# Kernel optimization log

Hardware: AMD Instinct MI355X
Metric: run time of the kernel (lower is better)

The kernel has to match this reference:

```python
import jax, jax.numpy as jnp
import numpy as np

B, S, D, H, DH = 2, 1024, 1024, 16, 64  # batch, seq, dim_model, heads, dim_head


def setup_inputs() -> dict:
    key = jax.random.key(0)
    ks = jax.random.split(key, 9)
    def W(k):
        return jax.random.normal(k, (D, D), jnp.float32) * 0.02
    z = jnp.zeros((D,), jnp.float32)
    return {
        "x": jax.random.normal(ks[0], (B, S, D), jnp.float32),
        "rel_pos_emb": jax.random.normal(ks[1], (B, S, D), jnp.float32),
        "padding_mask": jnp.zeros((B, S), jnp.int32),
        "Wq": W(ks[2]), "bq": z,
        "Wk": W(ks[3]), "bk": z,
        "Wv": W(ks[4]), "bv": z,
        "Wqr": W(ks[5]), "bqr": z,
        "Wkr": W(ks[6]), "bkr": z,
        "Wc": W(ks[7]), "bc": z,
    }


def reference(x, rel_pos_emb, padding_mask, Wq, bq, Wk, bk, Wv, bv, Wqr, bqr, Wkr, bkr, Wc, bc):
    b, s, d = x.shape

    def proj(t, W_, b_):  # (b,s,D) -> (b,H,s,DH)
        return (t @ W_.T + b_).reshape(b, s, H, DH).transpose(0, 2, 1, 3)

    q = proj(x, Wq, bq)
    k = proj(x, Wk, bk)
    v = proj(x, Wv, bv)
    qr = proj(rel_pos_emb, Wqr, bqr)
    kr = proj(rel_pos_emb, Wkr, bkr)

    # relative position index: clamp(i - j + MAX_REL_POS/2, 0, MAX_REL_POS-1), MAX_REL_POS = S
    idx = jnp.arange(s)
    pos = jnp.clip(idx[:, None] - idx[None, :] + s // 2, 0, s - 1)  # (s,s) int
    pos_b = jnp.broadcast_to(pos[None, None], (b, H, s, s))

    c2c = jnp.einsum('bhid,bhjd->bhij', q, k)
    c2p_att = jnp.einsum('bhid,bhjd->bhij', q, kr)
    c2p = jnp.take_along_axis(c2p_att, pos_b, axis=-1)   # gather along last dim
    p2c_att = jnp.einsum('bhid,bhjd->bhij', qr, k)
    p2c = jnp.take_along_axis(p2c_att, pos_b, axis=-2)   # gather along query dim

    scale = jnp.sqrt(jnp.asarray(3 * DH, jnp.float32))
    scores = (c2c + c2p + p2c) / scale
    scores = jnp.where(padding_mask[:, None, None, :] == 1, -jnp.inf, scores)
    attn = jax.nn.softmax(scores, axis=-1)  # dropout is identity in eval

    out = jnp.einsum('bhij,bhjd->bhid', attn, v)
    out = out.transpose(0, 2, 1, 3).reshape(b, s, H * DH)
    return out @ Wc.T + bc
```

## Files before the change

kernel.cpp:

```cpp
#include <hip/hip_runtime.h>

typedef unsigned short u16;
typedef unsigned int   u32;
typedef __bf16 bf16x8 __attribute__((ext_vector_type(8)));
typedef float  f32x4  __attribute__((ext_vector_type(4)));

__device__ __forceinline__ float b2f(u16 s) { return __uint_as_float(((u32)s) << 16); }
__device__ __forceinline__ u16 f2b(float f) {
  u32 x = __float_as_uint(f);
  return (u16)((x + 0x7FFFu + ((x >> 16) & 1u)) >> 16);
}

union U16x8 { uint4 u; u16 s[8]; };

__device__ __forceinline__ uint4 cvt8(const float4 a, const float4 b) {
  U16x8 r;
  r.s[0] = f2b(a.x); r.s[1] = f2b(a.y); r.s[2] = f2b(a.z); r.s[3] = f2b(a.w);
  r.s[4] = f2b(b.x); r.s[5] = f2b(b.y); r.s[6] = f2b(b.z); r.s[7] = f2b(b.w);
  return r.u;
}

typedef __attribute__((address_space(3))) u32 lds_u32;
typedef const __attribute__((address_space(1))) u32 glb_u32;
__device__ __forceinline__ void gld16(const u16* gp, u16* lp) {
  __builtin_amdgcn_global_load_lds((glb_u32*)gp, (lds_u32*)lp, 16, 0, 0);
}

struct CvtArgs { const float* s[8]; u16* d[8]; int n[8]; };

__global__ __launch_bounds__(256) void cvt_bf16(CvtArgs c) {
  const int t = blockIdx.y;
  const int i = (blockIdx.x * 256 + threadIdx.x) * 8;
  if (i >= c.n[t]) return;
  const float4 a = *(const float4*)(c.s[t] + i);
  const float4 b = *(const float4*)(c.s[t] + i + 4);
  *(uint4*)(c.d[t] + i) = cvt8(a, b);
}

struct GemmBArgs { const u16* A[5]; const u16* W[5]; const float* Bi[5]; void* C[5]; int vtz; };

template <int BN, bool OUT_F32>
__global__ __launch_bounds__(256) void gemm_lds(GemmBArgs g, int M, int N, int K) {
  const int z = blockIdx.z;
  const u16* __restrict__ A = g.A[z];
  const u16* __restrict__ W = g.W[z];
  const float* __restrict__ Bi = g.Bi[z];

  const int m0 = blockIdx.y * 128, n0 = blockIdx.x * BN;
  const int tid = threadIdx.x, wv = tid >> 6, lane = tid & 63;
  const int wm = wv >> 1, wn = wv & 1;
  const int lr = lane & 15, lq = lane >> 4;
  constexpr int NT = BN / 32;

  __shared__ u16 As[128 * 64];
  __shared__ u16 Ws[BN * 64];

  const f32x4 vzero = {0.f, 0.f, 0.f, 0.f};
  f32x4 acc[4][NT];
#pragma unroll
  for (int i = 0; i < 4; ++i)
#pragma unroll
    for (int j = 0; j < NT; ++j) acc[i][j] = vzero;

  const int srow = lane >> 3;
  const int sc   = (lane & 7) ^ srow;

  for (int kb = 0; kb < K; kb += 64) {
    __syncthreads();
#pragma unroll
    for (int t = 0; t < 4; ++t) {
      const u16* gp = A + (size_t)(m0 + t * 32 + wv * 8 + srow) * K + kb + sc * 8;
      gld16(gp, As + (t * 32 + wv * 8) * 64 + lane * 8);
    }
#pragma unroll
    for (int t = 0; t < NT; ++t) {
      const u16* gp = W + (size_t)(n0 + t * 32 + wv * 8 + srow) * K + kb + sc * 8;
      gld16(gp, Ws + (t * 32 + wv * 8) * 64 + lane * 8);
    }
    __syncthreads();
#pragma unroll
    for (int kk = 0; kk < 2; ++kk) {
      bf16x8 af[4], bw[NT];
#pragma unroll
      for (int mt = 0; mt < 4; ++mt) {
        const int row = wm * 64 + mt * 16 + lr;
        af[mt] = *(const bf16x8*)&As[row * 64 + (((kk << 2) | lq) ^ (row & 7)) * 8];
      }
#pragma unroll
      for (int nt = 0; nt < NT; ++nt) {
        const int row = wn * (BN / 2) + nt * 16 + lr;
        bw[nt] = *(const bf16x8*)&Ws[row * 64 + (((kk << 2) | lq) ^ (row & 7)) * 8];
      }
#pragma unroll
      for (int mt = 0; mt < 4; ++mt)
#pragma unroll
        for (int nt = 0; nt < NT; ++nt)
          acc[mt][nt] = __builtin_amdgcn_mfma_f32_16x16x32_bf16(af[mt], bw[nt], acc[mt][nt], 0, 0, 0);
    }
  }

#pragma unroll
  for (int mt = 0; mt < 4; ++mt) {
#pragma unroll
    for (int nt = 0; nt < NT; ++nt) {
      const int col = n0 + wn * (BN / 2) + nt * 16 + lr;
      const float bia = Bi[col];
      const int row0 = m0 + wm * 64 + mt * 16 + lq * 4;
      if (OUT_F32) {
#pragma unroll
        for (int r = 0; r < 4; ++r)
          ((float*)g.C[z])[(size_t)(row0 + r) * N + col] = acc[mt][nt][r] + bia;
      } else if (z == g.vtz) {
        ushort4 pk;
        pk.x = f2b(acc[mt][nt][0] + bia); pk.y = f2b(acc[mt][nt][1] + bia);
        pk.z = f2b(acc[mt][nt][2] + bia); pk.w = f2b(acc[mt][nt][3] + bia);
        const int bb = row0 >> 10, s0 = row0 & 1023;
        *(ushort4*)((u16*)g.C[z] + ((size_t)bb << 20) + ((size_t)col << 10) + s0) = pk;
      } else {
#pragma unroll
        for (int r = 0; r < 4; ++r)
          ((u16*)g.C[z])[(size_t)(row0 + r) * N + col] = f2b(acc[mt][nt][r] + bia);
      }
    }
  }
}

struct GemmArgs { const void* A[5]; const float* W[5]; const float* Bi[5]; void* C[5]; int vtz; };

template <bool A_F32, bool OUT_F32>
__global__ __launch_bounds__(256) void gemm5(GemmArgs g, int M, int N, int K) {
  const int z = blockIdx.z;
  const float* __restrict__ Wf = g.W[z];
  const float* __restrict__ Bi = g.Bi[z];

  const int m0 = blockIdx.y * 128, n0 = blockIdx.x * 128;
  const int tid = threadIdx.x;
  const int wv = tid >> 6, lane = tid & 63;
  const int wm = wv >> 1, wn = wv & 1;
  const int lr = lane & 15, lq = lane >> 4;

  __shared__ alignas(16) u16 As[128][64];
  __shared__ alignas(16) u16 Ws[128][64];

  const f32x4 vzero = {0.f, 0.f, 0.f, 0.f};
  f32x4 acc[4][4];
#pragma unroll
  for (int i = 0; i < 4; ++i)
#pragma unroll
    for (int j = 0; j < 4; ++j) acc[i][j] = vzero;

  const int srow = tid >> 1;
  const int sc0  = (tid & 1) * 32;
  const float* pw = Wf + (size_t)(n0 + srow) * K + sc0;
  const float* paf = A_F32 ? ((const float*)g.A[z] + (size_t)(m0 + srow) * K + sc0) : nullptr;
  const u16*   pab = A_F32 ? nullptr : ((const u16*)g.A[z] + (size_t)(m0 + srow) * K + sc0);

  for (int k0 = 0; k0 < K; k0 += 64) {
#pragma unroll
    for (int u_ = 0; u_ < 4; ++u_) {
      const float4 w0 = *(const float4*)(pw + k0 + u_ * 8);
      const float4 w1 = *(const float4*)(pw + k0 + u_ * 8 + 4);
      *(uint4*)&Ws[srow][sc0 + u_ * 8] = cvt8(w0, w1);
      if (A_F32) {
        const float4 a0 = *(const float4*)(paf + k0 + u_ * 8);
        const float4 a1 = *(const float4*)(paf + k0 + u_ * 8 + 4);
        *(uint4*)&As[srow][sc0 + u_ * 8] = cvt8(a0, a1);
      } else {
        *(uint4*)&As[srow][sc0 + u_ * 8] = *(const uint4*)(pab + k0 + u_ * 8);
      }
    }
    __syncthreads();
#pragma unroll
    for (int kk = 0; kk < 2; ++kk) {
      bf16x8 af[4], bfr[4];
#pragma unroll
      for (int mt = 0; mt < 4; ++mt)
        af[mt] = *(const bf16x8*)&As[wm * 64 + mt * 16 + lr][kk * 32 + lq * 8];
#pragma unroll
      for (int nt = 0; nt < 4; ++nt)
        bfr[nt] = *(const bf16x8*)&Ws[wn * 64 + nt * 16 + lr][kk * 32 + lq * 8];
#pragma unroll
      for (int mt = 0; mt < 4; ++mt)
#pragma unroll
        for (int nt = 0; nt < 4; ++nt)
          acc[mt][nt] = __builtin_amdgcn_mfma_f32_16x16x32_bf16(af[mt], bfr[nt], acc[mt][nt], 0, 0, 0);
    }
    __syncthreads();
  }

#pragma unroll
  for (int mt = 0; mt < 4; ++mt) {
#pragma unroll
    for (int nt = 0; nt < 4; ++nt) {
      const int col = n0 + wn * 64 + nt * 16 + lr;
      const float bia = Bi[col];
      const int row0 = m0 + wm * 64 + mt * 16 + lq * 4;
      if (OUT_F32) {
#pragma unroll
        for (int r = 0; r < 4; ++r)
          ((float*)g.C[z])[(size_t)(row0 + r) * N + col] = acc[mt][nt][r] + bia;
      } else if (z == g.vtz) {
        ushort4 pk;
        pk.x = f2b(acc[mt][nt][0] + bia); pk.y = f2b(acc[mt][nt][1] + bia);
        pk.z = f2b(acc[mt][nt][2] + bia); pk.w = f2b(acc[mt][nt][3] + bia);
        const int bb = row0 >> 10, s0 = row0 & 1023;
        *(ushort4*)((u16*)g.C[z] + ((size_t)bb << 20) + ((size_t)col << 10) + s0) = pk;
      } else {
#pragma unroll
        for (int r = 0; r < 4; ++r)
          ((u16*)g.C[z])[(size_t)(row0 + r) * N + col] = f2b(acc[mt][nt][r] + bia);
      }
    }
  }
}

__global__ __launch_bounds__(256, 2) void attn_wave(
    const u16* __restrict__ q, const u16* __restrict__ k,
    const u16* __restrict__ vT, const u16* __restrict__ qr,
    const u16* __restrict__ kr, const int* __restrict__ pmask,
    u16* __restrict__ ao) {
  constexpr int S = 1024, Dm = 1024;
  constexpr int GP = 37;
  constexpr int PBP = 36;
  constexpr int WLDS = 11776;

  __shared__ alignas(16) char smem[4 * WLDS];

  const int bx = blockIdx.x;
  const int bh = bx & 31, it = bx >> 5;
  const int bb = bh >> 4, h = bh & 15;
  const int i0 = it * 32;

  const int tid = threadIdx.x;
  const int wv = tid >> 6, lane = tid & 63;
  const int lq = lane >> 4, lr = lane & 15;

  char* wbase = smem + wv * WLDS;
  float* G1b = (float*)wbase;
  float* G2b = (float*)(wbase + 4736);
  u16*   Pb  = (u16*)(wbase + 9472);

  const u16* qb  = q  + ((size_t)bb << 20) + h * 64;
  const u16* kb  = k  + ((size_t)bb << 20) + h * 64;
  const u16* qrb = qr + ((size_t)bb << 20) + h * 64;
  const u16* krb = kr + ((size_t)bb << 20) + h * 64;
  const u16* vtb = vT + ((size_t)bb << 20) + ((size_t)h << 16);
  const int* pmb = pmask + ((size_t)bb << 10);

  const float kscale = 1.44269504088896f / 13.856406460551018f;

  bf16x8 qf[2][2];
#pragma unroll
  for (int mt = 0; mt < 2; ++mt)
#pragma unroll
    for (int kk = 0; kk < 2; ++kk)
      qf[mt][kk] = *(const bf16x8*)(qb + (size_t)(i0 + mt * 16 + lr) * Dm + kk * 32 + lq * 8);

  const f32x4 vzero = {0.f, 0.f, 0.f, 0.f};
  f32x4 o[2][4];
#pragma unroll
  for (int mt = 0; mt < 2; ++mt)
#pragma unroll
    for (int nd = 0; nd < 4; ++nd) o[mt][nd] = vzero;
  float mst[2][4], lst[2][4];
#pragma unroll
  for (int mt = 0; mt < 2; ++mt)
#pragma unroll
    for (int r = 0; r < 4; ++r) { mst[mt][r] = -1e30f; lst[mt][r] = 0.f; }

#pragma unroll 1
  for (int t8 = 0; t8 < 8; ++t8) {
    const int j0 = (wv + t8 * 4) * 32;
    const int pb_ = i0 - j0 + 481;

    bf16x8 kf[2][2], krf[4][2], vf[4];
#pragma unroll
    for (int nt = 0; nt < 2; ++nt) {
      const u16* kp = kb + (size_t)(j0 + nt * 16 + lr) * Dm + lq * 8;
      kf[nt][0] = *(const bf16x8*)kp;
      kf[nt][1] = *(const bf16x8*)(kp + 32);
    }
#pragma unroll
    for (int n4 = 0; n4 < 4; ++n4) {
      int p = pb_ + n4 * 16 + lr; p = p < 0 ? 0 : (p > 1023 ? 1023 : p);
      const u16* kp = krb + (size_t)p * Dm + lq * 8;
      krf[n4][0] = *(const bf16x8*)kp;
      krf[n4][1] = *(const bf16x8*)(kp + 32);
    }
#pragma unroll
    for (int n4 = 0; n4 < 4; ++n4)
      vf[n4] = *(const bf16x8*)(vtb + (size_t)(n4 * 16 + lr) * S + j0 + lq * 8);
    const int mv0 = pmb[j0 + lr], mv1 = pmb[j0 + 16 + lr];

    f32x4 cc[2][2];
#pragma unroll
    for (int mt = 0; mt < 2; ++mt)
#pragma unroll
      for (int nt = 0; nt < 2; ++nt) {
        f32x4 a = vzero;
        a = __builtin_amdgcn_mfma_f32_16x16x32_bf16(qf[mt][0], kf[nt][0], a, 0, 0, 0);
        a = __builtin_amdgcn_mfma_f32_16x16x32_bf16(qf[mt][1], kf[nt][1], a, 0, 0, 0);
        cc[mt][nt] = a;
      }

#pragma unroll
    for (int mt = 0; mt < 2; ++mt)
#pragma unroll
      for (int n4 = 0; n4 < 4; ++n4) {
        f32x4 a = vzero;
        a = __builtin_amdgcn_mfma_f32_16x16x32_bf16(qf[mt][0], krf[n4][0], a, 0, 0, 0);
        a = __builtin_amdgcn_mfma_f32_16x16x32_bf16(qf[mt][1], krf[n4][1], a, 0, 0, 0);
        const int t = n4 * 16 + lr;
#pragma unroll
        for (int r = 0; r < 4; ++r) {
          const int arow = mt * 16 + lq * 4 + r;
          const int u = t - arow;
          if ((unsigned)u < 32u) G1b[arow * GP + u] = a[r];
        }
      }

#pragma unroll
    for (int mt = 0; mt < 2; ++mt)
#pragma unroll
      for (int n4 = 0; n4 < 4; ++n4) {
        int p = pb_ + n4 * 16 + lr; p = p < 0 ? 0 : (p > 1023 ? 1023 : p);
        const u16* qp = qrb + (size_t)p * Dm + lq * 8;
        bf16x8 q0 = *(const bf16x8*)qp;
        bf16x8 q1 = *(const bf16x8*)(qp + 32);
        f32x4 a = vzero;
        a = __builtin_amdgcn_mfma_f32_16x16x32_bf16(kf[mt][0], q0, a, 0, 0, 0);
        a = __builtin_amdgcn_mfma_f32_16x16x32_bf16(kf[mt][1], q1, a, 0, 0, 0);
        const int t = n4 * 16 + lr;
#pragma unroll
        for (int r = 0; r < 4; ++r) {
          const int brow = mt * 16 + lq * 4 + r;
          const int u = t + brow - 31;
          if ((unsigned)u < 32u) G2b[brow * GP + u] = a[r];
        }
      }

    float pv[2][2][4], alpha[2][4];
#pragma unroll
    for (int mt = 0; mt < 2; ++mt) {
      float mx[4];
#pragma unroll
      for (int r = 0; r < 4; ++r) {
        const int a_ = mt * 16 + lq * 4 + r;
#pragma unroll
        for (int nt = 0; nt < 2; ++nt) {
          const int b_ = nt * 16 + lr;
          float s = cc[mt][nt][r] + G1b[a_ * GP + 31 - b_] + G2b[b_ * GP + a_];
          s *= kscale;
          if ((nt ? mv1 : mv0) != 0) s = -1e30f;
          pv[mt][nt][r] = s;
        }
        mx[r] = fmaxf(pv[mt][0][r], pv[mt][1][r]);
      }
#pragma unroll
      for (int r = 0; r < 4; ++r) {
        mx[r] = fmaxf(mx[r], __shfl_xor(mx[r], 1));
        mx[r] = fmaxf(mx[r], __shfl_xor(mx[r], 2));
        mx[r] = fmaxf(mx[r], __shfl_xor(mx[r], 4));
        mx[r] = fmaxf(mx[r], __shfl_xor(mx[r], 8));
        const float mnew = fmaxf(mst[mt][r], mx[r]);
        alpha[mt][r] = exp2f(mst[mt][r] - mnew);
        mst[mt][r] = mnew;
        float rs = 0.f;
#pragma unroll
        for (int nt = 0; nt < 2; ++nt) {
          const float p = exp2f(pv[mt][nt][r] - mnew);
          pv[mt][nt][r] = p;
          rs += p;
        }
        rs += __shfl_xor(rs, 1);
        rs += __shfl_xor(rs, 2);
        rs += __shfl_xor(rs, 4);
        rs += __shfl_xor(rs, 8);
        lst[mt][r] = lst[mt][r] * alpha[mt][r] + rs;
        const int a_ = mt * 16 + lq * 4 + r;
#pragma unroll
        for (int nt = 0; nt < 2; ++nt)
          Pb[a_ * PBP + nt * 16 + lr] = f2b(pv[mt][nt][r]);
      }
    }

#pragma unroll
    for (int mt = 0; mt < 2; ++mt)
#pragma unroll
      for (int nd = 0; nd < 4; ++nd)
#pragma unroll
        for (int r = 0; r < 4; ++r) o[mt][nd][r] *= alpha[mt][r];
#pragma unroll
    for (int mt = 0; mt < 2; ++mt) {
      union { uint2 u2[2]; bf16x8 v; } pr;
      const u16* prow = Pb + (mt * 16 + lr) * PBP + lq * 8;
      pr.u2[0] = *(const uint2*)prow;
      pr.u2[1] = *(const uint2*)(prow + 4);
#pragma unroll
      for (int nd = 0; nd < 4; ++nd)
        o[mt][nd] = __builtin_amdgcn_mfma_f32_16x16x32_bf16(pr.v, vf[nd], o[mt][nd], 0, 0, 0);
    }
  }

  {
    float* Orm = (float*)wbase;
    float* mlw = (float*)(wbase + 8192);
    float* llw = (float*)(wbase + 8320);
#pragma unroll
    for (int mt = 0; mt < 2; ++mt)
#pragma unroll
      for (int nd = 0; nd < 4; ++nd)
#pragma unroll
        for (int r = 0; r < 4; ++r)
          Orm[(mt * 16 + lq * 4 + r) * 64 + nd * 16 + lr] = o[mt][nd][r];
    if (lr == 0) {
#pragma unroll
      for (int mt = 0; mt < 2; ++mt)
#pragma unroll
        for (int r = 0; r < 4; ++r) {
          mlw[mt * 16 + lq * 4 + r] = mst[mt][r];
          llw[mt * 16 + lq * 4 + r] = lst[mt][r];
        }
    }
  }
  __syncthreads();
  {
    const int a_ = tid >> 3, d0 = (tid & 7) * 8;
    float Ms = -1e30f;
#pragma unroll
    for (int w = 0; w < 4; ++w)
      Ms = fmaxf(Ms, *(const float*)(smem + w * WLDS + 8192 + a_ * 4));
    float L = 0.f, acc[8];
#pragma unroll
    for (int d = 0; d < 8; ++d) acc[d] = 0.f;
#pragma unroll
    for (int w = 0; w < 4; ++w) {
      const char* wb = smem + w * WLDS;
      const float mw = *(const float*)(wb + 8192 + a_ * 4);
      const float lw = *(const float*)(wb + 8320 + a_ * 4);
      const float al = exp2f(mw - Ms);
      L += al * lw;
      const float* Ow = (const float*)wb + a_ * 64 + d0;
#pragma unroll
      for (int d = 0; d < 8; ++d) acc[d] += al * Ow[d];
    }
    const float inv = 1.f / L;
    U16x8 pk;
#pragma unroll
    for (int d = 0; d < 8; ++d) pk.s[d] = f2b(acc[d] * inv);
    *(uint4*)(ao + ((size_t)((bb << 10) + i0 + a_) << 10) + (h << 6) + d0) = pk.u;
  }
}

extern "C" void kernel_launch(void* const* d_in, const int* in_sizes, int n_in,
                              void* d_out, int out_size, void* d_ws, size_t ws_size,
                              hipStream_t stream) {
  const float* x   = (const float*)d_in[0];
  const float* rpe = (const float*)d_in[1];
  const int*   pm  = (const int*)d_in[2];
  const float* Wq  = (const float*)d_in[3];  const float* bq  = (const float*)d_in[4];
  const float* Wk  = (const float*)d_in[5];  const float* bk  = (const float*)d_in[6];
  const float* Wv  = (const float*)d_in[7];  const float* bv  = (const float*)d_in[8];
  const float* Wqr = (const float*)d_in[9];  const float* bqr = (const float*)d_in[10];
  const float* Wkr = (const float*)d_in[11]; const float* bkr = (const float*)d_in[12];
  const float* Wc  = (const float*)d_in[13]; const float* bc  = (const float*)d_in[14];

  const size_t NE = (size_t)2 * 1024 * 1024;
  const size_t WE = (size_t)1024 * 1024;
  u16* ws = (u16*)d_ws;

  if (ws_size >= (10 * NE + 6 * WE) * sizeof(u16)) {
    u16* q   = ws;          u16* k   = ws + NE;     u16* vT  = ws + 2 * NE;
    u16* qr  = ws + 3 * NE; u16* kr  = ws + 4 * NE;
    u16* xb  = ws + 5 * NE;
    u16* ao  = ws + 5 * NE;
    u16* rpb = ws + 6 * NE;
    u16* wb  = ws + 7 * NE;
    u16* Wqb = wb;           u16* Wkb = wb + WE;     u16* Wvb = wb + 2 * WE;
    u16* Wqrb= wb + 3 * WE;  u16* Wkrb= wb + 4 * WE; u16* Wcb = wb + 5 * WE;

    CvtArgs c;
    c.s[0] = x;   c.d[0] = xb;   c.n[0] = (int)NE;
    c.s[1] = rpe; c.d[1] = rpb;  c.n[1] = (int)NE;
    c.s[2] = Wq;  c.d[2] = Wqb;  c.n[2] = (int)WE;
    c.s[3] = Wk;  c.d[3] = Wkb;  c.n[3] = (int)WE;
    c.s[4] = Wv;  c.d[4] = Wvb;  c.n[4] = (int)WE;
    c.s[5] = Wqr; c.d[5] = Wqrb; c.n[5] = (int)WE;
    c.s[6] = Wkr; c.d[6] = Wkrb; c.n[6] = (int)WE;
    c.s[7] = Wc;  c.d[7] = Wcb;  c.n[7] = (int)WE;
    cvt_bf16<<<dim3(1024, 8), 256, 0, stream>>>(c);

    GemmBArgs g;
    g.A[0] = xb;  g.W[0] = Wqb;  g.Bi[0] = bq;  g.C[0] = q;
    g.A[1] = xb;  g.W[1] = Wkb;  g.Bi[1] = bk;  g.C[1] = k;
    g.A[2] = xb;  g.W[2] = Wvb;  g.Bi[2] = bv;  g.C[2] = vT;
    g.A[3] = rpb; g.W[3] = Wqrb; g.Bi[3] = bqr; g.C[3] = qr;
    g.A[4] = rpb; g.W[4] = Wkrb; g.Bi[4] = bkr; g.C[4] = kr;
    g.vtz = 2;
    gemm_lds<128, false><<<dim3(8, 16, 5), 256, 0, stream>>>(g, 2048, 1024, 1024);

    attn_wave<<<dim3(1024), 256, 0, stream>>>(q, k, vT, qr, kr, pm, ao);

    GemmBArgs g2;
    for (int i = 0; i < 5; ++i) { g2.A[i] = ao; g2.W[i] = Wcb; g2.Bi[i] = bc; g2.C[i] = d_out; }
    g2.vtz = -1;
    gemm_lds<64, true><<<dim3(16, 16, 1), 256, 0, stream>>>(g2, 2048, 1024, 1024);
  } else {
    if (ws_size < 6 * NE * sizeof(u16)) return;
    u16* q  = ws;          u16* k  = ws + NE;     u16* vT = ws + 2 * NE;
    u16* qr = ws + 3 * NE; u16* kr = ws + 4 * NE; u16* ao = ws + 5 * NE;

    GemmArgs g;
    g.A[0] = x;   g.W[0] = Wq;  g.Bi[0] = bq;  g.C[0] = q;
    g.A[1] = x;   g.W[1] = Wk;  g.Bi[1] = bk;  g.C[1] = k;
    g.A[2] = x;   g.W[2] = Wv;  g.Bi[2] = bv;  g.C[2] = vT;
    g.A[3] = rpe; g.W[3] = Wqr; g.Bi[3] = bqr; g.C[3] = qr;
    g.A[4] = rpe; g.W[4] = Wkr; g.Bi[4] = bkr; g.C[4] = kr;
    g.vtz = 2;
    gemm5<true, false><<<dim3(8, 16, 5), 256, 0, stream>>>(g, 2048, 1024, 1024);

    attn_wave<<<dim3(1024), 256, 0, stream>>>(q, k, vT, qr, kr, pm, ao);

    GemmArgs g2;
    for (int i = 0; i < 5; ++i) { g2.A[i] = ao; g2.W[i] = Wc; g2.Bi[i] = bc; g2.C[i] = d_out; }
    g2.vtz = -1;
    gemm5<false, true><<<dim3(8, 16, 1), 256, 0, stream>>>(g2, 2048, 1024, 1024);
  }
}
```

Before: 261.5 us.

## Store gathered relative-position scores in bf16 LDS and raise attention occupancy

The c2p/p2c staging buffers in shared memory now hold bf16 instead of fp32, which shrinks per-wave LDS. The launch bound is raised from 2 to 4 blocks per CU so more waves can hide latency. The kr fragment is now loaded per n4 iteration instead of prefetched into registers, which lowers register pressure. Clamping of position indices is skipped when the whole tile is in range. The cost is reduced precision in the positional score terms, and the tighter register budget may cause spills.

```diff
diff --git a/kernel.cpp b/kernel.cpp
--- a/kernel.cpp
+++ b/kernel.cpp
@@ -214,7 +214,7 @@
   }
 }
 
-__global__ __launch_bounds__(256, 2) void attn_wave(
+__global__ __launch_bounds__(256, 4) void attn_wave(
     const u16* __restrict__ q, const u16* __restrict__ k,
     const u16* __restrict__ vT, const u16* __restrict__ qr,
     const u16* __restrict__ kr, const int* __restrict__ pmask,
@@ -222,7 +222,7 @@
   constexpr int S = 1024, Dm = 1024;
   constexpr int GP = 37;
   constexpr int PBP = 36;
-  constexpr int WLDS = 11776;
+  constexpr int WLDS = 8448;
 
   __shared__ alignas(16) char smem[4 * WLDS];
 
@@ -236,9 +236,9 @@
   const int lq = lane >> 4, lr = lane & 15;
 
   char* wbase = smem + wv * WLDS;
-  float* G1b = (float*)wbase;
-  float* G2b = (float*)(wbase + 4736);
-  u16*   Pb  = (u16*)(wbase + 9472);
+  u16* G1b = (u16*)wbase;
+  u16* G2b = (u16*)(wbase + 2368);
+  u16* Pb  = (u16*)(wbase + 4736);
 
   const u16* qb  = q  + ((size_t)bb << 20) + h * 64;
   const u16* kb  = k  + ((size_t)bb << 20) + h * 64;
@@ -272,20 +272,14 @@
   for (int t8 = 0; t8 < 8; ++t8) {
     const int j0 = (wv + t8 * 4) * 32;
     const int pb_ = i0 - j0 + 481;
-
-    bf16x8 kf[2][2], krf[4][2], vf[4];
+    const bool noclamp = (pb_ >= 0) && (pb_ <= 1023 - 63);
+
+    bf16x8 kf[2][2], vf[4];
 #pragma unroll
     for (int nt = 0; nt < 2; ++nt) {
       const u16* kp = kb + (size_t)(j0 + nt * 16 + lr) * Dm + lq * 8;
       kf[nt][0] = *(const bf16x8*)kp;
       kf[nt][1] = *(const bf16x8*)(kp + 32);
-    }
-#pragma unroll
-    for (int n4 = 0; n4 < 4; ++n4) {
-      int p = pb_ + n4 * 16 + lr; p = p < 0 ? 0 : (p > 1023 ? 1023 : p);
-      const u16* kp = krb + (size_t)p * Dm + lq * 8;
-      krf[n4][0] = *(const bf16x8*)kp;
-      krf[n4][1] = *(const bf16x8*)(kp + 32);
     }
 #pragma unroll
     for (int n4 = 0; n4 < 4; ++n4)
@@ -304,40 +298,48 @@
       }
 
 #pragma unroll
-    for (int mt = 0; mt < 2; ++mt)
-#pragma unroll
-      for (int n4 = 0; n4 < 4; ++n4) {
+    for (int n4 = 0; n4 < 4; ++n4) {
+      int p = pb_ + n4 * 16 + lr;
+      if (!noclamp) p = p < 0 ? 0 : (p > 1023 ? 1023 : p);
+      const u16* kp = krb + (size_t)p * Dm + lq * 8;
+      const bf16x8 kr0 = *(const bf16x8*)kp;
+      const bf16x8 kr1 = *(const bf16x8*)(kp + 32);
+      const int t = n4 * 16 + lr;
+#pragma unroll
+      for (int mt = 0; mt < 2; ++mt) {
         f32x4 a = vzero;
-        a = __builtin_amdgcn_mfma_f32_16x16x32_bf16(qf[mt][0], krf[n4][0], a, 0, 0, 0);
-        a = __builtin_amdgcn_mfma_f32_16x16x32_bf16(qf[mt][1], krf[n4][1], a, 0, 0, 0);
-        const int t = n4 * 16 + lr;
+        a = __builtin_amdgcn_mfma_f32_16x16x32_bf16(qf[mt][0], kr0, a, 0, 0, 0);
+        a = __builtin_amdgcn_mfma_f32_16x16x32_bf16(qf[mt][1], kr1, a, 0, 0, 0);
 #pragma unroll
         for (int r = 0; r < 4; ++r) {
           const int arow = mt * 16 + lq * 4 + r;
           const int u = t - arow;
-          if ((unsigned)u < 32u) G1b[arow * GP + u] = a[r];
+          if ((unsigned)u < 32u) G1b[arow * GP + u] = f2b(a[r]);
         }
       }
-
-#pragma unroll
-    for (int mt = 0; mt < 2; ++mt)
-#pragma unroll
-      for (int n4 = 0; n4 < 4; ++n4) {
-        int p = pb_ + n4 * 16 + lr; p = p < 0 ? 0 : (p > 1023 ? 1023 : p);
-        const u16* qp = qrb + (size_t)p * Dm + lq * 8;
-        bf16x8 q0 = *(const bf16x8*)qp;
-        bf16x8 q1 = *(const bf16x8*)(qp + 32);
+    }
+
+#pragma unroll
+    for (int n4 = 0; n4 < 4; ++n4) {
+      int p = pb_ + n4 * 16 + lr;
+      if (!noclamp) p = p < 0 ? 0 : (p > 1023 ? 1023 : p);
+      const u16* qp = qrb + (size_t)p * Dm + lq * 8;
+      const bf16x8 q0 = *(const bf16x8*)qp;
+      const bf16x8 q1 = *(const bf16x8*)(qp + 32);
+      const int t = n4 * 16 + lr;
+#pragma unroll
+      for (int mt = 0; mt < 2; ++mt) {
         f32x4 a = vzero;
         a = __builtin_amdgcn_mfma_f32_16x16x32_bf16(kf[mt][0], q0, a, 0, 0, 0);
         a = __builtin_amdgcn_mfma_f32_16x16x32_bf16(kf[mt][1], q1, a, 0, 0, 0);
-        const int t = n4 * 16 + lr;
 #pragma unroll
         for (int r = 0; r < 4; ++r) {
           const int brow = mt * 16 + lq * 4 + r;
           const int u = t + brow - 31;
-          if ((unsigned)u < 32u) G2b[brow * GP + u] = a[r];
+          if ((unsigned)u < 32u) G2b[brow * GP + u] = f2b(a[r]);
         }
       }
+    }
 
     float pv[2][2][4], alpha[2][4];
 #pragma unroll
@@ -349,7 +351,7 @@
 #pragma unroll
         for (int nt = 0; nt < 2; ++nt) {
           const int b_ = nt * 16 + lr;
-          float s = cc[mt][nt][r] + G1b[a_ * GP + 31 - b_] + G2b[b_ * GP + a_];
+          float s = cc[mt][nt][r] + b2f(G1b[a_ * GP + 31 - b_]) + b2f(G2b[b_ * GP + a_]);
           s *= kscale;
           if ((nt ? mv1 : mv0) != 0) s = -1e30f;
           pv[mt][nt][r] = s;
```

Result: slower. 439.0 us (+67.9%).
